# Kernel optimization log

Measured on AMD Instinct MI355X. Metric: run time of the kernel, lower is better.

Reference implementation:

```python
import jax, jax.numpy as jnp
from jax import lax
import numpy as np


def _lstm_layer(x, Wih, Whh, bih, bhh):
    """Single-direction LSTM layer, PyTorch gate order (i, f, g, o).
    x: [B, T, D_in] -> hidden sequence [B, T, H]."""
    B, T, _ = x.shape
    H = Whh.shape[1]
    # Precompute input contribution for all timesteps: [B, T, 4H]
    xw = jnp.einsum('btd,gd->btg', x, Wih) + bih + bhh

    def step(carry, xt):
        h, c = carry
        gates = xt + h @ Whh.T  # [B, 4H]
        i, f, g, o = jnp.split(gates, 4, axis=-1)
        i = jax.nn.sigmoid(i)
        f = jax.nn.sigmoid(f)
        g = jnp.tanh(g)
        o = jax.nn.sigmoid(o)
        c = f * c + i * g
        h = o * jnp.tanh(c)
        return (h, c), h

    h0 = jnp.zeros((B, H), dtype=x.dtype)
    c0 = jnp.zeros((B, H), dtype=x.dtype)
    _, hs = lax.scan(step, (h0, c0), jnp.swapaxes(xw, 0, 1))  # [T, B, H]
    return jnp.swapaxes(hs, 0, 1)  # [B, T, H]


def setup_inputs() -> dict:
    key = jax.random.key(0)
    ks = jax.random.split(key, 9)
    B, T, D, H = 64, 2048, 256, 128
    s = 1.0 / np.sqrt(H)  # PyTorch uniform(-1/sqrt(H), 1/sqrt(H)) init scale
    u = lambda k, shp: jax.random.uniform(k, shp, jnp.float32, -s, s)
    return {
        'x': jax.random.normal(ks[0], (B, T, D), jnp.float32),
        'Wih0': u(ks[1], (4 * H, D)),
        'Whh0': u(ks[2], (4 * H, H)),
        'bih0': u(ks[3], (4 * H,)),
        'bhh0': u(ks[4], (4 * H,)),
        'Wih1': u(ks[5], (4 * H, H)),
        'Whh1': u(ks[6], (4 * H, H)),
        'bih1': u(ks[7], (4 * H,)),
        'bhh1': u(ks[8], (4 * H,)),
    }


def reference(x, Wih0, Whh0, bih0, bhh0, Wih1, Whh1, bih1, bhh1):
    # 2-layer stacked LSTM; inter-layer dropout (p=0.1) is identity at eval.
    h1 = _lstm_layer(x, Wih0, Whh0, bih0, bhh0)
    h2 = _lstm_layer(h1, Wih1, Whh1, bih1, bhh1)
    return h2
```

## Files before the change

### kernel.cpp

```cpp
#include <hip/hip_runtime.h>
#include <hip/hip_bf16.h>

#define H 128
#define FOURH 512
#define BATCH 64
#define SEQ 2048
#define TC SEQ
#define NCHUNK 128
#define RS 64
#define GSTRIDE (BATCH * FOURH)

typedef _Float16 half8 __attribute__((ext_vector_type(8)));
typedef float f32x4 __attribute__((ext_vector_type(4)));

__global__ void prep_kernel(const float* __restrict__ Wih0,
                            const float* __restrict__ bih0, const float* __restrict__ bhh0,
                            const float* __restrict__ bih1, const float* __restrict__ bhh1,
                            const float* __restrict__ Wih1,
                            float* __restrict__ Wt0,
                            float* __restrict__ b0, float* __restrict__ b1,
                            _Float16* __restrict__ wt1h,
                            int* __restrict__ flags) {
    int id = blockIdx.x * 256 + threadIdx.x;
    const int N0 = 256 * 512;
    if (id < N0) {
        int k = id >> 9, n = id & 511;
        Wt0[id] = Wih0[n * 256 + k];
    } else if (id < N0 + 512) {
        int i = id - N0;
        b0[i] = bih0[i] + bhh0[i];
    } else if (id < N0 + 1024) {
        int i = id - (N0 + 512);
        b1[i] = bih1[i] + bhh1[i];
    } else if (id < N0 + 1024 + 65536) {
        int i = id - (N0 + 1024);
        wt1h[i] = (_Float16)Wih1[i];
    } else if (id < N0 + 1024 + 65536 + 272) {
        flags[id - (N0 + 1024 + 65536)] = 0;
    }
}

__device__ __forceinline__ float sigmoid_f(float x) {
    return __builtin_amdgcn_rcpf(1.f + __expf(-x));
}
__device__ __forceinline__ float tanh_f(float x) {
    return 1.f - 2.f * __builtin_amdgcn_rcpf(__expf(2.f * x) + 1.f);
}

#define LDS_BARRIER()                                                \
    do {                                                             \
        asm volatile("s_waitcnt lgkmcnt(0)" ::: "memory");           \
        __builtin_amdgcn_s_barrier();                                \
        __builtin_amdgcn_sched_barrier(0);                           \
    } while (0)

#define BM 128
#define BN 128
#define BK 32

__global__ __launch_bounds__(512, 2) void lstm_fused_kernel(
    const float* __restrict__ x,
    const float* __restrict__ Wt0,
    const float* __restrict__ b0sum,
    float* __restrict__ gring,
    const float* __restrict__ Whh0,
    const _Float16* __restrict__ wt1h,
    const float* __restrict__ Whh1,
    const float* __restrict__ b1,
    _Float16* __restrict__ h1p,
    float* __restrict__ g1r,
    float* __restrict__ out,
    int* __restrict__ flags)
{
    const int tid = threadIdx.x;

    int* prodF     = flags;
    int* consF     = flags + 8;
    int* chunkDone = flags + 16;
    int* g1Done    = flags + 144;

    __shared__ _Float16 hbuf[2][8][136];
    __shared__ float As[BK][BM + 4];
    __shared__ float Bs[BK][BN];

    if (blockIdx.x >= 16) {
        const int j   = blockIdx.x - 16;
        const int sub = j & 31;
        const int cls = j >> 5;
        const int by  = sub >> 2;
        const int bx  = sub & 3;
        const int n0  = bx * BN;

        if (cls < 5) {
            const int tm  = tid >> 5;
            const int tn  = tid & 31;
            int ar[2], aq[2], bkk[2], bq[2];
#pragma unroll
            for (int l2 = 0; l2 < 2; ++l2) {
                int fidx = tid + l2 * 512;
                ar[l2] = fidx >> 3; aq[l2] = fidx & 7;
                bkk[l2] = fidx >> 5; bq[l2] = fidx & 31;
            }
            float4 bvg = *(const float4*)&b0sum[n0 + tn * 4];

            for (int idx = cls; idx < NCHUNK; idx += 5) {
                if (idx >= 4) {
                    if (tid == 0) {
                        while (__hip_atomic_load(&prodF[by], __ATOMIC_RELAXED,
                                                 __HIP_MEMORY_SCOPE_AGENT) < 16 * (idx - 3))
                            __builtin_amdgcn_s_sleep(4);
                    }
                    __syncthreads();
                }
                const float* aptr[2];
#pragma unroll
                for (int l2 = 0; l2 < 2; ++l2) {
                    int rl = by * BM + ar[l2];
                    int b = rl >> 4;
                    int t = idx * 16 + (rl & 15);
                    aptr[l2] = x + ((size_t)b * SEQ + t) * 256 + aq[l2] * 4;
                }
                float acc[2][4][4];
#pragma unroll
                for (int rh = 0; rh < 2; ++rh)
#pragma unroll
                    for (int i = 0; i < 4; ++i)
#pragma unroll
                        for (int jj = 0; jj < 4; ++jj) acc[rh][i][jj] = 0.f;

                for (int k0 = 0; k0 < 256; k0 += BK) {
                    __syncthreads();
#pragma unroll
                    for (int l2 = 0; l2 < 2; ++l2) {
                        float4 v = *(const float4*)(aptr[l2] + k0);
                        As[aq[l2] * 4 + 0][ar[l2]] = v.x;
                        As[aq[l2] * 4 + 1][ar[l2]] = v.y;
                        As[aq[l2] * 4 + 2][ar[l2]] = v.z;
                        As[aq[l2] * 4 + 3][ar[l2]] = v.w;
                    }
#pragma unroll
                    for (int l2 = 0; l2 < 2; ++l2) {
                        float4 v = *(const float4*)(Wt0 + (size_t)(k0 + bkk[l2]) * FOURH + n0 + bq[l2] * 4);
                        *(float4*)&Bs[bkk[l2]][bq[l2] * 4] = v;
                    }
                    __syncthreads();
#pragma unroll
                    for (int kk = 0; kk < BK; ++kk) {
                        float a[8], bb[4];
                        *(float4*)&a[0] = *(const float4*)&As[kk][tm * 4];
                        *(float4*)&a[4] = *(const float4*)&As[kk][64 + tm * 4];
                        *(float4*)&bb[0] = *(const float4*)&Bs[kk][tn * 4];
#pragma unroll
                        for (int rh = 0; rh < 2; ++rh)
#pragma unroll
                            for (int i = 0; i < 4; ++i)
#pragma unroll
                                for (int jj = 0; jj < 4; ++jj)
                                    acc[rh][i][jj] = fmaf(a[rh * 4 + i], bb[jj], acc[rh][i][jj]);
                    }
                }
#pragma unroll
                for (int rh = 0; rh < 2; ++rh)
#pragma unroll
                    for (int i = 0; i < 4; ++i) {
                        int rl = by * BM + rh * 64 + tm * 4 + i;
                        int b = rl >> 4;
                        int slot = (idx & 3) * 16 + (rl & 15);
                        float* gp = gring + ((size_t)slot * BATCH + b) * FOURH + n0 + tn * 4;
                        float4 o = make_float4(acc[rh][i][0] + bvg.x, acc[rh][i][1] + bvg.y,
                                               acc[rh][i][2] + bvg.z, acc[rh][i][3] + bvg.w);
                        *(float4*)gp = o;
                    }
                __syncthreads();
                if (tid == 0) {
                    __threadfence();
                    __hip_atomic_fetch_add(&chunkDone[idx], 1, __ATOMIC_RELEASE,
                                           __HIP_MEMORY_SCOPE_AGENT);
                }
            }
        } else {
            const int wv  = tid >> 6;
            const int l   = tid & 63;
            const int li  = l & 15;
            const int q   = l >> 4;
            const int gb1 = 8 * by + wv;

            float bv1g[8];
#pragma unroll
            for (int ct = 0; ct < 8; ++ct) bv1g[ct] = b1[n0 + ct * 16 + li];

            for (int m = cls - 5; m < NCHUNK; m += 2) {
                if (tid == 0) {
                    while (__hip_atomic_load(&prodF[by], __ATOMIC_RELAXED,
                                             __HIP_MEMORY_SCOPE_AGENT) < 16 * (m + 1))
                        __builtin_amdgcn_s_sleep(4);
                    if (m >= 4) {
                        while (__hip_atomic_load(&consF[by], __ATOMIC_RELAXED,
                                                 __HIP_MEMORY_SCOPE_AGENT) < 16 * (m - 3))
                            __builtin_amdgcn_s_sleep(4);
                    }
                    (void)__hip_atomic_load(&prodF[by], __ATOMIC_ACQUIRE,
                                            __HIP_MEMORY_SCOPE_AGENT);
                }
                __syncthreads();

                const int t0 = m * 16;
                half8 Af[4];
                const _Float16* ap = h1p + ((size_t)(t0 + li) * BATCH + gb1) * H + q * 8;
#pragma unroll
                for (int kf = 0; kf < 4; ++kf)
                    Af[kf] = *(const half8*)(ap + kf * 32);

                f32x4 acc1[8];
#pragma unroll
                for (int ct = 0; ct < 8; ++ct) {
                    acc1[ct][0] = bv1g[ct]; acc1[ct][1] = bv1g[ct];
                    acc1[ct][2] = bv1g[ct]; acc1[ct][3] = bv1g[ct];
                }
#pragma unroll
                for (int ct = 0; ct < 8; ++ct) {
                    const _Float16* wp = wt1h + (size_t)(n0 + ct * 16 + li) * H + q * 8;
#pragma unroll
                    for (int kf = 0; kf < 4; ++kf) {
                        half8 Bfr = *(const half8*)(wp + kf * 32);
                        acc1[ct] = __builtin_amdgcn_mfma_f32_16x16x32_f16(Af[kf], Bfr, acc1[ct], 0, 0, 0);
                    }
                }
                const int srow = (m & 3) * 16 + q * 4;
#pragma unroll
                for (int ct = 0; ct < 8; ++ct)
#pragma unroll
                    for (int i = 0; i < 4; ++i)
                        g1r[((size_t)(srow + i) * BATCH + gb1) * FOURH + n0 + ct * 16 + li] = acc1[ct][i];
                __syncthreads();
                if (tid == 0) {
                    __threadfence();
                    __hip_atomic_fetch_add(&g1Done[m], 1, __ATOMIC_RELEASE,
                                           __HIP_MEMORY_SCOPE_AGENT);
                }
            }
        }
        return;
    }

    const int w  = tid >> 6;
    const int l  = tid & 63;
    const int li = l & 15;
    const int q  = l >> 4;
    const int u  = 16 * w + li;
    const int b0 = q * 2;
    const int ab = ((li >> 2) * 2) + (li & 1);

#define WAIT_FLAG(ptr, tgtv)                                                   \
    do {                                                                       \
        if (tid == 0) {                                                        \
            while (__hip_atomic_load((ptr), __ATOMIC_RELAXED,                  \
                                     __HIP_MEMORY_SCOPE_AGENT) < (tgtv))       \
                __builtin_amdgcn_s_sleep(4);                                   \
            (void)__hip_atomic_load((ptr), __ATOMIC_ACQUIRE,                   \
                                    __HIP_MEMORY_SCOPE_AGENT);                 \
        }                                                                      \
        __syncthreads();                                                       \
    } while (0)

#define SCAN_STEP(S, PB, GR, GBASE, BOFF0, BOFF1, BFARR, STORE_STMT)              \
    {                                                                             \
        half8 Afr[4];                                                             \
        _Pragma("unroll")                                                         \
        for (int kf = 0; kf < 4; ++kf)                                            \
            Afr[kf] = *(const half8*)&hbuf[PB][ab][kf * 32 + q * 8];              \
        f32x4 acc[4];                                                             \
        _Pragma("unroll")                                                         \
        for (int tl = 0; tl < 4; ++tl) {                                          \
            acc[tl][0] = GR[tl * 2 + 0]; acc[tl][1] = GR[tl * 2 + 1];             \
            acc[tl][2] = 0.f;            acc[tl][3] = 0.f;                        \
        }                                                                         \
        {                                                                         \
            const float* gp_ = (GBASE) + (size_t)(((S) + 4) & (RS - 1)) * GSTRIDE; \
            _Pragma("unroll")                                                     \
            for (int tl = 0; tl < 4; ++tl) {                                      \
                GR[tl * 2 + 0] = gp_[(BOFF0) + tl * H];                           \
                GR[tl * 2 + 1] = gp_[(BOFF1) + tl * H];                           \
            }                                                                     \
        }                                                                         \
        _Pragma("unroll")                                                         \
        for (int kf = 0; kf < 4; ++kf)                                            \
            _Pragma("unroll")                                                     \
            for (int tl = 0; tl < 4; ++tl)                                        \
                acc[tl] = __builtin_amdgcn_mfma_f32_16x16x32_f16(Afr[kf], BFARR[tl][kf], acc[tl], 0, 0, 0); \
        {                                                                         \
            float ig = sigmoid_f(acc[0][0]);                                      \
            float fg = sigmoid_f(acc[1][0]);                                      \
            float gg = tanh_f(acc[2][0]);                                         \
            float og = sigmoid_f(acc[3][0]);                                      \
            c0 = fmaf(fg, c0, ig * gg);                                           \
            h0 = og * tanh_f(c0);                                                 \
            float ig1 = sigmoid_f(acc[0][1]);                                     \
            float fg1 = sigmoid_f(acc[1][1]);                                     \
            float gg1 = tanh_f(acc[2][1]);                                        \
            float og1 = sigmoid_f(acc[3][1]);                                     \
            c1 = fmaf(fg1, c1, ig1 * gg1);                                        \
            h1v = og1 * tanh_f(c1);                                               \
        }                                                                         \
        hbuf[PB ^ 1][b0][u]     = (_Float16)h0;                                   \
        hbuf[PB ^ 1][b0 + 1][u] = (_Float16)h1v;                                  \
        STORE_STMT                                                                \
        LDS_BARRIER();                                                            \
    }

    if (blockIdx.x < 8) {
        const int g = blockIdx.x;

        half8 Bf[4][4];
#pragma unroll
        for (int tl = 0; tl < 4; ++tl)
#pragma unroll
            for (int kf = 0; kf < 4; ++kf) {
                const float* wp = Whh0 + (size_t)(tl * 128 + u) * H + kf * 32 + q * 8;
                float4 v0 = *(const float4*)wp;
                float4 v1 = *(const float4*)(wp + 4);
                half8 b;
                b[0] = (_Float16)v0.x; b[1] = (_Float16)v0.y;
                b[2] = (_Float16)v0.z; b[3] = (_Float16)v0.w;
                b[4] = (_Float16)v1.x; b[5] = (_Float16)v1.y;
                b[6] = (_Float16)v1.z; b[7] = (_Float16)v1.w;
                Bf[tl][kf] = b;
            }

        float c0 = 0.f, c1 = 0.f, h0 = 0.f, h1v = 0.f;
        hbuf[0][b0][u]     = (_Float16)0.f;
        hbuf[0][b0 + 1][u] = (_Float16)0.f;

        const int boff0 = (8 * g + b0) * FOURH + u;
        const int boff1 = boff0 + FOURH;

        WAIT_FLAG(&chunkDone[0], 32);

        float Ga[8], Gb[8], Gc[8], Gd[8];
#pragma unroll
        for (int tl = 0; tl < 4; ++tl) {
            Ga[tl * 2 + 0] = gring[(size_t)0 * GSTRIDE + boff0 + tl * H];
            Ga[tl * 2 + 1] = gring[(size_t)0 * GSTRIDE + boff1 + tl * H];
            Gb[tl * 2 + 0] = gring[(size_t)1 * GSTRIDE + boff0 + tl * H];
            Gb[tl * 2 + 1] = gring[(size_t)1 * GSTRIDE + boff1 + tl * H];
            Gc[tl * 2 + 0] = gring[(size_t)2 * GSTRIDE + boff0 + tl * H];
            Gc[tl * 2 + 1] = gring[(size_t)2 * GSTRIDE + boff1 + tl * H];
            Gd[tl * 2 + 0] = gring[(size_t)3 * GSTRIDE + boff0 + tl * H];
            Gd[tl * 2 + 1] = gring[(size_t)3 * GSTRIDE + boff1 + tl * H];
        }

        _Float16* php = h1p + (size_t)(8 * g + b0) * H + u;

#define P_STORE { php[0] = (_Float16)h0; php[128] = (_Float16)h1v; php += BATCH * H; }

        for (int s4 = 0; s4 < TC; s4 += 4) {
            if ((s4 & 15) == 0) {
                int k = (s4 >> 4) + 1;
                if (k > NCHUNK - 1) k = NCHUNK - 1;
                WAIT_FLAG(&chunkDone[k], 32);
            }
            SCAN_STEP(s4 + 0, 0, Ga, gring, boff0, boff1, Bf, P_STORE)
            SCAN_STEP(s4 + 1, 1, Gb, gring, boff0, boff1, Bf, P_STORE)
            SCAN_STEP(s4 + 2, 0, Gc, gring, boff0, boff1, Bf, P_STORE)
            SCAN_STEP(s4 + 3, 1, Gd, gring, boff0, boff1, Bf, P_STORE)
            if ((s4 & 15) == 12) {
                __threadfence();
                __syncthreads();
                if (tid == 0)
                    __hip_atomic_store(&prodF[g], s4 + 4, __ATOMIC_RELEASE,
                                       __HIP_MEMORY_SCOPE_AGENT);
            }
        }
#undef P_STORE
    } else {
        const int g = blockIdx.x - 8;

        half8 Bf[4][4];
#pragma unroll
        for (int tl = 0; tl < 4; ++tl)
#pragma unroll
            for (int kf = 0; kf < 4; ++kf) {
                const float* wp = Whh1 + (size_t)(tl * 128 + u) * H + kf * 32 + q * 8;
                float4 v0 = *(const float4*)wp;
                float4 v1 = *(const float4*)(wp + 4);
                half8 b;
                b[0] = (_Float16)v0.x; b[1] = (_Float16)v0.y;
                b[2] = (_Float16)v0.z; b[3] = (_Float16)v0.w;
                b[4] = (_Float16)v1.x; b[5] = (_Float16)v1.y;
                b[6] = (_Float16)v1.z; b[7] = (_Float16)v1.w;
                Bf[tl][kf] = b;
            }

        float c0 = 0.f, c1 = 0.f, h0, h1v;
        hbuf[0][b0][u]     = (_Float16)0.f;
        hbuf[0][b0 + 1][u] = (_Float16)0.f;

        const int boff0 = (8 * g + b0) * FOURH + u;
        const int boff1 = boff0 + FOURH;
        float* op0 = out + (size_t)(8 * g + b0) * SEQ * H + u;
        float* op1 = out + (size_t)(8 * g + b0 + 1) * SEQ * H + u;

        WAIT_FLAG(&g1Done[0], 32);

        float Ga[8], Gb[8], Gc[8], Gd[8];
#pragma unroll
        for (int tl = 0; tl < 4; ++tl) {
            Ga[tl * 2 + 0] = g1r[(size_t)0 * GSTRIDE + boff0 + tl * H];
            Ga[tl * 2 + 1] = g1r[(size_t)0 * GSTRIDE + boff1 + tl * H];
            Gb[tl * 2 + 0] = g1r[(size_t)1 * GSTRIDE + boff0 + tl * H];
            Gb[tl * 2 + 1] = g1r[(size_t)1 * GSTRIDE + boff1 + tl * H];
            Gc[tl * 2 + 0] = g1r[(size_t)2 * GSTRIDE + boff0 + tl * H];
            Gc[tl * 2 + 1] = g1r[(size_t)2 * GSTRIDE + boff1 + tl * H];
            Gd[tl * 2 + 0] = g1r[(size_t)3 * GSTRIDE + boff0 + tl * H];
            Gd[tl * 2 + 1] = g1r[(size_t)3 * GSTRIDE + boff1 + tl * H];
        }

#define C_STORE { op0[0] = h0; op1[0] = h1v; op0 += H; op1 += H; }

        for (int s4 = 0; s4 < TC; s4 += 4) {
            if ((s4 & 15) == 0) {
                int k = (s4 >> 4) + 1;
                if (k > NCHUNK - 1) k = NCHUNK - 1;
                WAIT_FLAG(&g1Done[k], 32);
            }
            SCAN_STEP(s4 + 0, 0, Ga, g1r, boff0, boff1, Bf, C_STORE)
            SCAN_STEP(s4 + 1, 1, Gb, g1r, boff0, boff1, Bf, C_STORE)
            SCAN_STEP(s4 + 2, 0, Gc, g1r, boff0, boff1, Bf, C_STORE)
            SCAN_STEP(s4 + 3, 1, Gd, g1r, boff0, boff1, Bf, C_STORE)
            if ((s4 & 15) == 12) {
                if (tid == 0)
                    __hip_atomic_store(&consF[g], s4 + 4, __ATOMIC_RELEASE,
                                       __HIP_MEMORY_SCOPE_AGENT);
            }
        }
#undef C_STORE
    }
#undef WAIT_FLAG
#undef SCAN_STEP
}

extern "C" void kernel_launch(void* const* d_in, const int* in_sizes, int n_in,
                              void* d_out, int out_size, void* d_ws, size_t ws_size,
                              hipStream_t stream) {
    const float* x    = (const float*)d_in[0];
    const float* Wih0 = (const float*)d_in[1];
    const float* Whh0 = (const float*)d_in[2];
    const float* bih0 = (const float*)d_in[3];
    const float* bhh0 = (const float*)d_in[4];
    const float* Wih1 = (const float*)d_in[5];
    const float* Whh1 = (const float*)d_in[6];
    const float* bih1 = (const float*)d_in[7];
    const float* bhh1 = (const float*)d_in[8];
    float* out = (float*)d_out;

    char* ws = (char*)d_ws;
    size_t off = 0;
    auto carve = [&](size_t bytes) -> char* {
        char* p = ws + off;
        off += (bytes + 255) & ~(size_t)255;
        return p;
    };

    float*     Wt0   = (float*)carve(256 * 512 * 4);
    float*     b0v   = (float*)carve(512 * 4);
    float*     b1v   = (float*)carve(512 * 4);
    _Float16*  wt1h  = (_Float16*)carve(65536 * 2);
    _Float16*  h1p   = (_Float16*)carve((size_t)SEQ * BATCH * H * 2);
    int*       flags = (int*)carve(272 * 4);
    float*     gring = (float*)carve((size_t)RS * GSTRIDE * 4);
    float*     g1r   = (float*)carve((size_t)RS * GSTRIDE * 4);

    prep_kernel<<<774, 256, 0, stream>>>(Wih0, bih0, bhh0, bih1, bhh1, Wih1,
                                         Wt0, b0v, b1v, wt1h, flags);

    lstm_fused_kernel<<<240, 512, 0, stream>>>(x, Wt0, b0v, gring,
                                               Whh0, wt1h, Whh1, b1v,
                                               h1p, g1r, out, flags);
}
```

Baseline: 2.495 ms.

## Replace bounded gate rings with full-sequence buffer and drop consumer backpressure

The two 64-slot ring buffers for layer-0 and layer-1 gate pre-activations become one full-sequence buffer. The layer-1 input projection writes its results in place over layer-0 entries that have already been consumed. With every step having its own slot, the consumer-progress flags and the producer waits on them are removed, so the input-projection blocks can run ahead of the recurrent scans instead of stalling on ring space. The cost is a much larger workspace (about 256 MB), so gate data is unlikely to stay cache-resident. Correctness now depends on the ordering between the layer-0 scan's reads and the layer-1 projection's overwrites of the same slots.

```diff
diff --git a/kernel.cpp b/kernel.cpp
--- a/kernel.cpp
+++ b/kernel.cpp
@@ -7,7 +7,6 @@
 #define SEQ 2048
 #define TC SEQ
 #define NCHUNK 128
-#define RS 64
 #define GSTRIDE (BATCH * FOURH)
 
 typedef _Float16 half8 __attribute__((ext_vector_type(8)));
@@ -62,26 +61,89 @@
     const float* __restrict__ x,
     const float* __restrict__ Wt0,
     const float* __restrict__ b0sum,
-    float* __restrict__ gring,
+    float* __restrict__ Gbuf,
     const float* __restrict__ Whh0,
     const _Float16* __restrict__ wt1h,
     const float* __restrict__ Whh1,
     const float* __restrict__ b1,
     _Float16* __restrict__ h1p,
-    float* __restrict__ g1r,
     float* __restrict__ out,
     int* __restrict__ flags)
 {
     const int tid = threadIdx.x;
 
     int* prodF     = flags;
-    int* consF     = flags + 8;
     int* chunkDone = flags + 16;
     int* g1Done    = flags + 144;
 
     __shared__ _Float16 hbuf[2][8][136];
     __shared__ float As[BK][BM + 4];
     __shared__ float Bs[BK][BN];
+
+    if (blockIdx.x >= 176) {
+        const int j   = blockIdx.x - 176;
+        const int sub = j & 31;
+        const int cls = j >> 5;
+        const int by  = sub >> 2;
+        const int bx  = sub & 3;
+        const int n0  = bx * BN;
+        const int wv  = tid >> 6;
+        const int l   = tid & 63;
+        const int li  = l & 15;
+        const int q   = l >> 4;
+        const int gb1 = 8 * by + wv;
+
+        float bv1g[8];
+#pragma unroll
+        for (int ct = 0; ct < 8; ++ct) bv1g[ct] = b1[n0 + ct * 16 + li];
+
+        for (int m = cls; m < NCHUNK; m += 2) {
+            if (tid == 0) {
+                while (__hip_atomic_load(&prodF[by], __ATOMIC_RELAXED,
+                                         __HIP_MEMORY_SCOPE_AGENT) < 16 * (m + 1))
+                    __builtin_amdgcn_s_sleep(4);
+                (void)__hip_atomic_load(&prodF[by], __ATOMIC_ACQUIRE,
+                                        __HIP_MEMORY_SCOPE_AGENT);
+            }
+            __syncthreads();
+
+            const int t0 = m * 16;
+            half8 Af[4];
+            const _Float16* ap = h1p + ((size_t)(t0 + li) * BATCH + gb1) * H + q * 8;
+#pragma unroll
+            for (int kf = 0; kf < 4; ++kf)
+                Af[kf] = *(const half8*)(ap + kf * 32);
+
+            f32x4 acc1[8];
+#pragma unroll
+            for (int ct = 0; ct < 8; ++ct) {
+                acc1[ct][0] = bv1g[ct]; acc1[ct][1] = bv1g[ct];
+                acc1[ct][2] = bv1g[ct]; acc1[ct][3] = bv1g[ct];
+            }
+#pragma unroll
+            for (int ct = 0; ct < 8; ++ct) {
+                const _Float16* wp = wt1h + (size_t)(n0 + ct * 16 + li) * H + q * 8;
+#pragma unroll
+                for (int kf = 0; kf < 4; ++kf) {
+                    half8 Bfr = *(const half8*)(wp + kf * 32);
+                    acc1[ct] = __builtin_amdgcn_mfma_f32_16x16x32_f16(Af[kf], Bfr, acc1[ct], 0, 0, 0);
+                }
+            }
+            const int srow = t0 + q * 4;
+#pragma unroll
+            for (int ct = 0; ct < 8; ++ct)
+#pragma unroll
+                for (int i = 0; i < 4; ++i)
+                    Gbuf[((size_t)(srow + i) * BATCH + gb1) * FOURH + n0 + ct * 16 + li] = acc1[ct][i];
+            __syncthreads();
+            if (tid == 0) {
+                __threadfence();
+                __hip_atomic_fetch_add(&g1Done[m], 1, __ATOMIC_RELEASE,
+                                       __HIP_MEMORY_SCOPE_AGENT);
+            }
+        }
+        return;
+    }
 
     if (blockIdx.x >= 16) {
         const int j   = blockIdx.x - 16;
@@ -90,154 +152,83 @@
         const int by  = sub >> 2;
         const int bx  = sub & 3;
         const int n0  = bx * BN;
-
-        if (cls < 5) {
-            const int tm  = tid >> 5;
-            const int tn  = tid & 31;
-            int ar[2], aq[2], bkk[2], bq[2];
+        const int tm  = tid >> 5;
+        const int tn  = tid & 31;
+
+        int ar[2], aq[2], bkk[2], bq[2];
+#pragma unroll
+        for (int l2 = 0; l2 < 2; ++l2) {
+            int fidx = tid + l2 * 512;
+            ar[l2] = fidx >> 3; aq[l2] = fidx & 7;
+            bkk[l2] = fidx >> 5; bq[l2] = fidx & 31;
+        }
+        float4 bvg = *(const float4*)&b0sum[n0 + tn * 4];
+
+        for (int idx = cls; idx < NCHUNK; idx += 5) {
+            const float* aptr[2];
 #pragma unroll
             for (int l2 = 0; l2 < 2; ++l2) {
-                int fidx = tid + l2 * 512;
-                ar[l2] = fidx >> 3; aq[l2] = fidx & 7;
-                bkk[l2] = fidx >> 5; bq[l2] = fidx & 31;
-            }
-            float4 bvg = *(const float4*)&b0sum[n0 + tn * 4];
-
-            for (int idx = cls; idx < NCHUNK; idx += 5) {
-                if (idx >= 4) {
-                    if (tid == 0) {
-                        while (__hip_atomic_load(&prodF[by], __ATOMIC_RELAXED,
-                                                 __HIP_MEMORY_SCOPE_AGENT) < 16 * (idx - 3))
-                            __builtin_amdgcn_s_sleep(4);
-                    }
-                    __syncthreads();
+                int rl = by * BM + ar[l2];
+                int b = rl >> 4;
+                int t = idx * 16 + (rl & 15);
+                aptr[l2] = x + ((size_t)b * SEQ + t) * 256 + aq[l2] * 4;
+            }
+            float acc[2][4][4];
+#pragma unroll
+            for (int rh = 0; rh < 2; ++rh)
+#pragma unroll
+                for (int i = 0; i < 4; ++i)
+#pragma unroll
+                    for (int jj = 0; jj < 4; ++jj) acc[rh][i][jj] = 0.f;
+
+            for (int k0 = 0; k0 < 256; k0 += BK) {
+                __syncthreads();
+#pragma unroll
+                for (int l2 = 0; l2 < 2; ++l2) {
+                    float4 v = *(const float4*)(aptr[l2] + k0);
+                    As[aq[l2] * 4 + 0][ar[l2]] = v.x;
+                    As[aq[l2] * 4 + 1][ar[l2]] = v.y;
+                    As[aq[l2] * 4 + 2][ar[l2]] = v.z;
+                    As[aq[l2] * 4 + 3][ar[l2]] = v.w;
                 }
-                const float* aptr[2];
 #pragma unroll
                 for (int l2 = 0; l2 < 2; ++l2) {
-                    int rl = by * BM + ar[l2];
+                    float4 v = *(const float4*)(Wt0 + (size_t)(k0 + bkk[l2]) * FOURH + n0 + bq[l2] * 4);
+                    *(float4*)&Bs[bkk[l2]][bq[l2] * 4] = v;
+                }
+                __syncthreads();
+#pragma unroll
+                for (int kk = 0; kk < BK; ++kk) {
+                    float a[8], bb[4];
+                    *(float4*)&a[0] = *(const float4*)&As[kk][tm * 4];
+                    *(float4*)&a[4] = *(const float4*)&As[kk][64 + tm * 4];
+                    *(float4*)&bb[0] = *(const float4*)&Bs[kk][tn * 4];
+#pragma unroll
+                    for (int rh = 0; rh < 2; ++rh)
+#pragma unroll
+                        for (int i = 0; i < 4; ++i)
+#pragma unroll
+                            for (int jj = 0; jj < 4; ++jj)
+                                acc[rh][i][jj] = fmaf(a[rh * 4 + i], bb[jj], acc[rh][i][jj]);
+                }
+            }
+#pragma unroll
+            for (int rh = 0; rh < 2; ++rh)
+#pragma unroll
+                for (int i = 0; i < 4; ++i) {
+                    int rl = by * BM + rh * 64 + tm * 4 + i;
                     int b = rl >> 4;
                     int t = idx * 16 + (rl & 15);
-                    aptr[l2] = x + ((size_t)b * SEQ + t) * 256 + aq[l2] * 4;
+                    float* gp = Gbuf + ((size_t)t * BATCH + b) * FOURH + n0 + tn * 4;
+                    float4 o = make_float4(acc[rh][i][0] + bvg.x, acc[rh][i][1] + bvg.y,
+                                           acc[rh][i][2] + bvg.z, acc[rh][i][3] + bvg.w);
+                    *(float4*)gp = o;
                 }
-                float acc[2][4][4];
-#pragma unroll
-                for (int rh = 0; rh < 2; ++rh)
-#pragma unroll
-                    for (int i = 0; i < 4; ++i)
-#pragma unroll
-                        for (int jj = 0; jj < 4; ++jj) acc[rh][i][jj] = 0.f;
-
-                for (int k0 = 0; k0 < 256; k0 += BK) {
-                    __syncthreads();
-#pragma unroll
-                    for (int l2 = 0; l2 < 2; ++l2) {
-                        float4 v = *(const float4*)(aptr[l2] + k0);
-                        As[aq[l2] * 4 + 0][ar[l2]] = v.x;
-                        As[aq[l2] * 4 + 1][ar[l2]] = v.y;
-                        As[aq[l2] * 4 + 2][ar[l2]] = v.z;
-                        As[aq[l2] * 4 + 3][ar[l2]] = v.w;
-                    }
-#pragma unroll
-                    for (int l2 = 0; l2 < 2; ++l2) {
-                        float4 v = *(const float4*)(Wt0 + (size_t)(k0 + bkk[l2]) * FOURH + n0 + bq[l2] * 4);
-                        *(float4*)&Bs[bkk[l2]][bq[l2] * 4] = v;
-                    }
-                    __syncthreads();
-#pragma unroll
-                    for (int kk = 0; kk < BK; ++kk) {
-                        float a[8], bb[4];
-                        *(float4*)&a[0] = *(const float4*)&As[kk][tm * 4];
-                        *(float4*)&a[4] = *(const float4*)&As[kk][64 + tm * 4];
-                        *(float4*)&bb[0] = *(const float4*)&Bs[kk][tn * 4];
-#pragma unroll
-                        for (int rh = 0; rh < 2; ++rh)
-#pragma unroll
-                            for (int i = 0; i < 4; ++i)
-#pragma unroll
-                                for (int jj = 0; jj < 4; ++jj)
-                                    acc[rh][i][jj] = fmaf(a[rh * 4 + i], bb[jj], acc[rh][i][jj]);
-                    }
-                }
-#pragma unroll
-                for (int rh = 0; rh < 2; ++rh)
-#pragma unroll
-                    for (int i = 0; i < 4; ++i) {
-                        int rl = by * BM + rh * 64 + tm * 4 + i;
-                        int b = rl >> 4;
-                        int slot = (idx & 3) * 16 + (rl & 15);
-                        float* gp = gring + ((size_t)slot * BATCH + b) * FOURH + n0 + tn * 4;
-                        float4 o = make_float4(acc[rh][i][0] + bvg.x, acc[rh][i][1] + bvg.y,
-                                               acc[rh][i][2] + bvg.z, acc[rh][i][3] + bvg.w);
-                        *(float4*)gp = o;
-                    }
-                __syncthreads();
-                if (tid == 0) {
-                    __threadfence();
-                    __hip_atomic_fetch_add(&chunkDone[idx], 1, __ATOMIC_RELEASE,
-                                           __HIP_MEMORY_SCOPE_AGENT);
-                }
-            }
-        } else {
-            const int wv  = tid >> 6;
-            const int l   = tid & 63;
-            const int li  = l & 15;
-            const int q   = l >> 4;
-            const int gb1 = 8 * by + wv;
-
-            float bv1g[8];
-#pragma unroll
-            for (int ct = 0; ct < 8; ++ct) bv1g[ct] = b1[n0 + ct * 16 + li];
-
-            for (int m = cls - 5; m < NCHUNK; m += 2) {
-                if (tid == 0) {
-                    while (__hip_atomic_load(&prodF[by], __ATOMIC_RELAXED,
-                                             __HIP_MEMORY_SCOPE_AGENT) < 16 * (m + 1))
-                        __builtin_amdgcn_s_sleep(4);
-                    if (m >= 4) {
-                        while (__hip_atomic_load(&consF[by], __ATOMIC_RELAXED,
-                                                 __HIP_MEMORY_SCOPE_AGENT) < 16 * (m - 3))
-                            __builtin_amdgcn_s_sleep(4);
-                    }
-                    (void)__hip_atomic_load(&prodF[by], __ATOMIC_ACQUIRE,
-                                            __HIP_MEMORY_SCOPE_AGENT);
-                }
-                __syncthreads();
-
-                const int t0 = m * 16;
-                half8 Af[4];
-                const _Float16* ap = h1p + ((size_t)(t0 + li) * BATCH + gb1) * H + q * 8;
-#pragma unroll
-                for (int kf = 0; kf < 4; ++kf)
-                    Af[kf] = *(const half8*)(ap + kf * 32);
-
-                f32x4 acc1[8];
-#pragma unroll
-                for (int ct = 0; ct < 8; ++ct) {
-                    acc1[ct][0] = bv1g[ct]; acc1[ct][1] = bv1g[ct];
-                    acc1[ct][2] = bv1g[ct]; acc1[ct][3] = bv1g[ct];
-                }
-#pragma unroll
-                for (int ct = 0; ct < 8; ++ct) {
-                    const _Float16* wp = wt1h + (size_t)(n0 + ct * 16 + li) * H + q * 8;
-#pragma unroll
-                    for (int kf = 0; kf < 4; ++kf) {
-                        half8 Bfr = *(const half8*)(wp + kf * 32);
-                        acc1[ct] = __builtin_amdgcn_mfma_f32_16x16x32_f16(Af[kf], Bfr, acc1[ct], 0, 0, 0);
-                    }
-                }
-                const int srow = (m & 3) * 16 + q * 4;
-#pragma unroll
-                for (int ct = 0; ct < 8; ++ct)
-#pragma unroll
-                    for (int i = 0; i < 4; ++i)
-                        g1r[((size_t)(srow + i) * BATCH + gb1) * FOURH + n0 + ct * 16 + li] = acc1[ct][i];
-                __syncthreads();
-                if (tid == 0) {
-                    __threadfence();
-                    __hip_atomic_fetch_add(&g1Done[m], 1, __ATOMIC_RELEASE,
-                                           __HIP_MEMORY_SCOPE_AGENT);
-                }
+            __syncthreads();
+            if (tid == 0) {
+                __threadfence();
+                __hip_atomic_fetch_add(&chunkDone[idx], 1, __ATOMIC_RELEASE,
+                                       __HIP_MEMORY_SCOPE_AGENT);
             }
         }
         return;
@@ -263,7 +254,7 @@
         __syncthreads();                                                       \
     } while (0)
 
-#define SCAN_STEP(S, PB, GR, GBASE, BOFF0, BOFF1, BFARR, STORE_STMT)              \
+#define SCAN_STEP(S, PB, GR, BFARR, STORE_STMT)                                   \
     {                                                                             \
         half8 Afr[4];                                                             \
         _Pragma("unroll")                                                         \
@@ -276,11 +267,12 @@
             acc[tl][2] = 0.f;            acc[tl][3] = 0.f;                        \
         }                                                                         \
         {                                                                         \
-            const float* gp_ = (GBASE) + (size_t)(((S) + 4) & (RS - 1)) * GSTRIDE; \
+            int sl_ = (S) + 4; if (sl_ > TC - 1) sl_ = TC - 1;                    \
+            const float* gp_ = Gbuf + (size_t)sl_ * GSTRIDE;                      \
             _Pragma("unroll")                                                     \
             for (int tl = 0; tl < 4; ++tl) {                                      \
-                GR[tl * 2 + 0] = gp_[(BOFF0) + tl * H];                           \
-                GR[tl * 2 + 1] = gp_[(BOFF1) + tl * H];                           \
+                GR[tl * 2 + 0] = gp_[boff0 + tl * H];                             \
+                GR[tl * 2 + 1] = gp_[boff1 + tl * H];                             \
             }                                                                     \
         }                                                                         \
         _Pragma("unroll")                                                         \
@@ -308,9 +300,11 @@
         LDS_BARRIER();                                                            \
     }
 
+    const int g = (blockIdx.x < 8) ? blockIdx.x : blockIdx.x - 8;
+    const int boff0 = (8 * g + b0) * FOURH + u;
+    const int boff1 = boff0 + FOURH;
+
     if (blockIdx.x < 8) {
-        const int g = blockIdx.x;
-
         half8 Bf[4][4];
 #pragma unroll
         for (int tl = 0; tl < 4; ++tl)
@@ -331,22 +325,19 @@
         hbuf[0][b0][u]     = (_Float16)0.f;
         hbuf[0][b0 + 1][u] = (_Float16)0.f;
 
-        const int boff0 = (8 * g + b0) * FOURH + u;
-        const int boff1 = boff0 + FOURH;
-
         WAIT_FLAG(&chunkDone[0], 32);
 
         float Ga[8], Gb[8], Gc[8], Gd[8];
 #pragma unroll
         for (int tl = 0; tl < 4; ++tl) {
-            Ga[tl * 2 + 0] = gring[(size_t)0 * GSTRIDE + boff0 + tl * H];
-            Ga[tl * 2 + 1] = gring[(size_t)0 * GSTRIDE + boff1 + tl * H];
-            Gb[tl * 2 + 0] = gring[(size_t)1 * GSTRIDE + boff0 + tl * H];
-            Gb[tl * 2 + 1] = gring[(size_t)1 * GSTRIDE + boff1 + tl * H];
-            Gc[tl * 2 + 0] = gring[(size_t)2 * GSTRIDE + boff0 + tl * H];
-            Gc[tl * 2 + 1] = gring[(size_t)2 * GSTRIDE + boff1 + tl * H];
-            Gd[tl * 2 + 0] = gring[(size_t)3 * GSTRIDE + boff0 + tl * H];
-            Gd[tl * 2 + 1] = gring[(size_t)3 * GSTRIDE + boff1 + tl * H];
+            Ga[tl * 2 + 0] = Gbuf[(size_t)0 * GSTRIDE + boff0 + tl * H];
+            Ga[tl * 2 + 1] = Gbuf[(size_t)0 * GSTRIDE + boff1 + tl * H];
+            Gb[tl * 2 + 0] = Gbuf[(size_t)1 * GSTRIDE + boff0 + tl * H];
+            Gb[tl * 2 + 1] = Gbuf[(size_t)1 * GSTRIDE + boff1 + tl * H];
+            Gc[tl * 2 + 0] = Gbuf[(size_t)2 * GSTRIDE + boff0 + tl * H];
+            Gc[tl * 2 + 1] = Gbuf[(size_t)2 * GSTRIDE + boff1 + tl * H];
+            Gd[tl * 2 + 0] = Gbuf[(size_t)3 * GSTRIDE + boff0 + tl * H];
+            Gd[tl * 2 + 1] = Gbuf[(size_t)3 * GSTRIDE + boff1 + tl * H];
         }
 
         _Float16* php = h1p + (size_t)(8 * g + b0) * H + u;
@@ -359,10 +350,10 @@
                 if (k > NCHUNK - 1) k = NCHUNK - 1;
                 WAIT_FLAG(&chunkDone[k], 32);
             }
-            SCAN_STEP(s4 + 0, 0, Ga, gring, boff0, boff1, Bf, P_STORE)
-            SCAN_STEP(s4 + 1, 1, Gb, gring, boff0, boff1, Bf, P_STORE)
-            SCAN_STEP(s4 + 2, 0, Gc, gring, boff0, boff1, Bf, P_STORE)
-            SCAN_STEP(s4 + 3, 1, Gd, gring, boff0, boff1, Bf, P_STORE)
+            SCAN_STEP(s4 + 0, 0, Ga, Bf, P_STORE)
+            SCAN_STEP(s4 + 1, 1, Gb, Bf, P_STORE)
+            SCAN_STEP(s4 + 2, 0, Gc, Bf, P_STORE)
+            SCAN_STEP(s4 + 3, 1, Gd, Bf, P_STORE)
             if ((s4 & 15) == 12) {
                 __threadfence();
                 __syncthreads();
@@ -373,8 +364,6 @@
         }
 #undef P_STORE
     } else {
-        const int g = blockIdx.x - 8;
-
         half8 Bf[4][4];
 #pragma unroll
         for (int tl = 0; tl < 4; ++tl)
@@ -395,24 +384,23 @@
         hbuf[0][b0][u]     = (_Float16)0.f;
         hbuf[0][b0 + 1][u] = (_Float16)0.f;
 
-        const int boff0 = (8 * g + b0) * FOURH + u;
-        const int boff1 = boff0 + FOURH;
         float* op0 = out + (size_t)(8 * g + b0) * SEQ * H + u;
         float* op1 = out + (size_t)(8 * g + b0 + 1) * SEQ * H + u;
 
+        WAIT_FLAG(&prodF[g], 96);
         WAIT_FLAG(&g1Done[0], 32);
 
         float Ga[8], Gb[8], Gc[8], Gd[8];
 #pragma unroll
         for (int tl = 0; tl < 4; ++tl) {
-            Ga[tl * 2 + 0] = g1r[(size_t)0 * GSTRIDE + boff0 + tl * H];
-            Ga[tl * 2 + 1] = g1r[(size_t)0 * GSTRIDE + boff1 + tl * H];
-            Gb[tl * 2 + 0] = g1r[(size_t)1 * GSTRIDE + boff0 + tl * H];
-            Gb[tl * 2 + 1] = g1r[(size_t)1 * GSTRIDE + boff1 + tl * H];
-            Gc[tl * 2 + 0] = g1r[(size_t)2 * GSTRIDE + boff0 + tl * H];
-            Gc[tl * 2 + 1] = g1r[(size_t)2 * GSTRIDE + boff1 + tl * H];
-            Gd[tl * 2 + 0] = g1r[(size_t)3 * GSTRIDE + boff0 + tl * H];
-            Gd[tl * 2 + 1] = g1r[(size_t)3 * GSTRIDE + boff1 + tl * H];
+            Ga[tl * 2 + 0] = Gbuf[(size_t)0 * GSTRIDE + boff0 + tl * H];
+            Ga[tl * 2 + 1] = Gbuf[(size_t)0 * GSTRIDE + boff1 + tl * H];
+            Gb[tl * 2 + 0] = Gbuf[(size_t)1 * GSTRIDE + boff0 + tl * H];
+            Gb[tl * 2 + 1] = Gbuf[(size_t)1 * GSTRIDE + boff1 + tl * H];
+            Gc[tl * 2 + 0] = Gbuf[(size_t)2 * GSTRIDE + boff0 + tl * H];
+            Gc[tl * 2 + 1] = Gbuf[(size_t)2 * GSTRIDE + boff1 + tl * H];
+            Gd[tl * 2 + 0] = Gbuf[(size_t)3 * GSTRIDE + boff0 + tl * H];
+            Gd[tl * 2 + 1] = Gbuf[(size_t)3 * GSTRIDE + boff1 + tl * H];
         }
 
 #define C_STORE { op0[0] = h0; op1[0] = h1v; op0 += H; op1 += H; }
@@ -423,15 +411,10 @@
                 if (k > NCHUNK - 1) k = NCHUNK - 1;
                 WAIT_FLAG(&g1Done[k], 32);
             }
-            SCAN_STEP(s4 + 0, 0, Ga, g1r, boff0, boff1, Bf, C_STORE)
-            SCAN_STEP(s4 + 1, 1, Gb, g1r, boff0, boff1, Bf, C_STORE)
-            SCAN_STEP(s4 + 2, 0, Gc, g1r, boff0, boff1, Bf, C_STORE)
-            SCAN_STEP(s4 + 3, 1, Gd, g1r, boff0, boff1, Bf, C_STORE)
-            if ((s4 & 15) == 12) {
-                if (tid == 0)
-                    __hip_atomic_store(&consF[g], s4 + 4, __ATOMIC_RELEASE,
-                                       __HIP_MEMORY_SCOPE_AGENT);
-            }
+            SCAN_STEP(s4 + 0, 0, Ga, Bf, C_STORE)
+            SCAN_STEP(s4 + 1, 1, Gb, Bf, C_STORE)
+            SCAN_STEP(s4 + 2, 0, Gc, Bf, C_STORE)
+            SCAN_STEP(s4 + 3, 1, Gd, Bf, C_STORE)
         }
 #undef C_STORE
     }
@@ -467,13 +450,12 @@
     _Float16*  wt1h  = (_Float16*)carve(65536 * 2);
     _Float16*  h1p   = (_Float16*)carve((size_t)SEQ * BATCH * H * 2);
     int*       flags = (int*)carve(272 * 4);
-    float*     gring = (float*)carve((size_t)RS * GSTRIDE * 4);
-    float*     g1r   = (float*)carve((size_t)RS * GSTRIDE * 4);
+    float*     gbuf  = (float*)carve((size_t)SEQ * GSTRIDE * 4);
 
     prep_kernel<<<774, 256, 0, stream>>>(Wih0, bih0, bhh0, bih1, bhh1, Wih1,
                                          Wt0, b0v, b1v, wt1h, flags);
 
-    lstm_fused_kernel<<<240, 512, 0, stream>>>(x, Wt0, b0v, gring,
+    lstm_fused_kernel<<<240, 512, 0, stream>>>(x, Wt0, b0v, gbuf,
                                                Whh0, wt1h, Whh1, b1v,
-                                               h1p, g1r, out, flags);
+                                               h1p, out, flags);
 }
```

Result: no change. 2.498 ms (+0.1%).
